# Performance work log

Hardware: AMD Instinct MI355X
Metric: run time of the kernel (lower is better)

The kernel has to match this reference:

```python
import math
import jax, jax.numpy as jnp
import numpy as np

B, S, E, H = 2, 2048, 1024, 16
D = E // H  # head_dim = 64
NEG = jnp.float32(-1e9)  # finite stand-in for masked_fill(-inf) to avoid NaN in attn @ V


def setup_inputs() -> dict:
    key = jax.random.key(0)
    ks = jax.random.split(key, 8)
    inp = {
        "query": jax.random.normal(ks[0], (B, S, E), jnp.float32),
        "key": jax.random.normal(ks[1], (B, S, E), jnp.float32),
        "value": jax.random.normal(ks[2], (B, S, E), jnp.float32),
        "Wq": jax.random.normal(ks[3], (E, E), jnp.float32) * 0.02,
        "bq": jnp.zeros((E,), jnp.float32),
        "Wk": jax.random.normal(ks[4], (E, E), jnp.float32) * 0.02,
        "bk": jnp.zeros((E,), jnp.float32),
        "Wv": jax.random.normal(ks[5], (E, E), jnp.float32) * 0.02,
        "bv": jnp.zeros((E,), jnp.float32),
        "pos_bias": jax.random.normal(ks[6], (H, 2 * S - 1), jnp.float32) * 0.02,
    }
    # gather indices: per-head row index [H,1,1] and relative-position index [S,S]
    inp["idx0"] = jnp.arange(H, dtype=jnp.int32).reshape(H, 1, 1)
    rel = np.arange(S)[:, None] - np.arange(S)[None, :] + (S - 1)  # in [0, 2S-2]
    inp["idx1"] = jnp.asarray(rel, jnp.int32)
    # causal boolean mask: True where masked (j > i)
    inp["mask"] = jnp.triu(jnp.ones((S, S), jnp.bool_), k=1)
    return inp


def _split(x):  # [B,S,E] -> [B,H,S,D]
    return x.reshape(B, S, H, D).transpose(0, 2, 1, 3)


def reference(query, key, value, Wq, bq, Wk, bk, Wv, bv, pos_bias, idx0, idx1, mask):
    q = _split(query @ Wq.T + bq)
    k = _split(key @ Wk.T + bk)
    v = _split(value @ Wv.T + bv)
    logits = jnp.einsum("bhqd,bhkd->bhqk", q, k) / math.sqrt(D)  # [B,H,S,S]
    logits = logits + pos_bias[idx0, idx1]  # gather -> [H,S,S], broadcast over B
    logits = jnp.where(mask, NEG, logits)   # masked_fill
    attn = jax.nn.log_softmax(logits, axis=-1)  # module uses LogSoftmax (faithful)
    out = jnp.einsum("bhqk,bhkd->bhqd", attn, v)
    return out.transpose(0, 2, 1, 3).reshape(B, S, E)
```

## Files before the change

### kernel.cpp

```cpp
#include <hip/hip_runtime.h>
#include <math.h>

constexpr int BB = 2;
constexpr int SS = 2048;
constexpr int EE = 1024;
constexpr int HH = 16;
constexpr int DD = 64;
constexpr int NSEG = 32;

typedef short short8 __attribute__((ext_vector_type(8)));
typedef short short4_t __attribute__((ext_vector_type(4)));
typedef float floatx4 __attribute__((ext_vector_type(4)));
typedef unsigned short ushort_t;

__device__ __forceinline__ ushort_t f2bf(float f) {
    unsigned int u = __float_as_uint(f);
    u += 0x7fffu + ((u >> 16) & 1u);
    return (ushort_t)(u >> 16);
}

__device__ __forceinline__ void gl_lds16(const void* g, void* l) {
    __builtin_amdgcn_global_load_lds(
        (const __attribute__((address_space(1))) void*)g,
        (__attribute__((address_space(3))) void*)l, 16, 0, 0);
}

__global__ __launch_bounds__(256) void repack_kernel(
    const float* __restrict__ s0, const float* __restrict__ s1, const float* __restrict__ s2,
    ushort_t* __restrict__ dst, int rows)
{
    const float* src = (blockIdx.z == 0) ? s0 : (blockIdx.z == 1) ? s1 : s2;
    ushort_t* d = dst + (size_t)blockIdx.z * rows * EE;
    const int idx = blockIdx.x * 256 + threadIdx.x;
    const int row = idx >> 7;
    const int gir = idx & 127;
    const int blk = gir >> 3, g = gir & 7;
    const int gp = g ^ (row & 7);
    const float* sp = src + (size_t)row * EE + gir * 8;
    float4 a = *(const float4*)sp;
    float4 b = *(const float4*)(sp + 4);
    short8 o;
    o[0] = (short)f2bf(a.x); o[1] = (short)f2bf(a.y); o[2] = (short)f2bf(a.z); o[3] = (short)f2bf(a.w);
    o[4] = (short)f2bf(b.x); o[5] = (short)f2bf(b.y); o[6] = (short)f2bf(b.z); o[7] = (short)f2bf(b.w);
    *(short8*)&d[(size_t)row * EE + blk * 64 + gp * 8] = o;
}

__global__ __launch_bounds__(256) void proj_kernel(
    const ushort_t* __restrict__ Xall, const ushort_t* __restrict__ Wall,
    const float* __restrict__ bq, const float* __restrict__ bk, const float* __restrict__ bv,
    ushort_t* __restrict__ qb, ushort_t* __restrict__ kbb,
    float* __restrict__ vf, ushort_t* __restrict__ vtb)
{
    __shared__ __align__(16) ushort_t Xs[128 * 64];
    __shared__ __align__(16) ushort_t Ws[128 * 64];

    const int z = blockIdx.z;
    const ushort_t* X = Xall + (size_t)z * BB * SS * EE;
    const ushort_t* W = Wall + (size_t)z * EE * EE;
    const float* bias = (z == 0) ? bq : (z == 1) ? bk : bv;

    const int t = threadIdx.x, w = t >> 6, l = t & 63, ln = t & 15, qd = (t >> 4) & 3;
    const int row0 = blockIdx.x * 128;
    const int col0 = blockIdx.y * 128;
    const int wzm = (w & 1) * 64, wzn = (w >> 1) * 64;

    floatx4 acc[4][4];
    #pragma unroll
    for (int i = 0; i < 4; ++i)
        #pragma unroll
        for (int j = 0; j < 4; ++j)
            acc[i][j] = (floatx4){0.f, 0.f, 0.f, 0.f};

    for (int k0 = 0; k0 < EE; k0 += 64) {
        __syncthreads();
        #pragma unroll
        for (int j = 0; j < 4; ++j) {
            const int c = w * 4 + j;
            const int r = c * 8 + (l >> 3);
            gl_lds16(&X[(size_t)(row0 + r) * EE + k0 + (l & 7) * 8], &Xs[c * 512]);
            gl_lds16(&W[(size_t)(col0 + r) * EE + k0 + (l & 7) * 8], &Ws[c * 512]);
        }
        __syncthreads();

        const ushort_t* Am = (z < 2) ? Ws : Xs;
        const ushort_t* Bn = (z < 2) ? Xs : Ws;
        #pragma unroll
        for (int kh = 0; kh < 2; ++kh) {
            const int sw = ((kh * 4 + qd) ^ (ln & 7)) * 8;
            short8 af[4], bfr[4];
            #pragma unroll
            for (int mi = 0; mi < 4; ++mi)
                af[mi] = *(const short8*)&Am[(wzm + mi * 16 + ln) * 64 + sw];
            #pragma unroll
            for (int ni = 0; ni < 4; ++ni)
                bfr[ni] = *(const short8*)&Bn[(wzn + ni * 16 + ln) * 64 + sw];
            #pragma unroll
            for (int mi = 0; mi < 4; ++mi)
                #pragma unroll
                for (int ni = 0; ni < 4; ++ni)
                    acc[mi][ni] = __builtin_amdgcn_mfma_f32_16x16x32_bf16(af[mi], bfr[ni], acc[mi][ni], 0, 0, 0);
        }
    }

    if (z < 2) {
        ushort_t* dst = z ? kbb : qb;
        #pragma unroll
        for (int mi = 0; mi < 4; ++mi) {
            const int o0 = col0 + wzm + mi * 16 + qd * 4;
            const float4 b4 = *(const float4*)&bias[o0];
            const int h = o0 >> 6, d0 = o0 & 63;
            const int g = d0 >> 3, dlow = d0 & 7;
            #pragma unroll
            for (int ni = 0; ni < 4; ++ni) {
                const int s = row0 + wzn + ni * 16 + ln;
                const int b = s >> 11, sr = s & (SS - 1);
                const int gp = g ^ (sr & 7);
                short4_t pk;
                pk[0] = (short)f2bf(acc[mi][ni][0] + b4.x);
                pk[1] = (short)f2bf(acc[mi][ni][1] + b4.y);
                pk[2] = (short)f2bf(acc[mi][ni][2] + b4.z);
                pk[3] = (short)f2bf(acc[mi][ni][3] + b4.w);
                *(short4_t*)&dst[((size_t)((b * HH + h) * SS) + sr) * DD + gp * 8 + dlow] = pk;
            }
        }
    } else {
        #pragma unroll
        for (int mi = 0; mi < 4; ++mi) {
            const int s0 = row0 + wzm + mi * 16 + qd * 4;
            const int b = s0 >> 11, sr0 = s0 & (SS - 1);
            const int sg = (sr0 >> 3) & 7, slow = sr0 & 7;
            #pragma unroll
            for (int ni = 0; ni < 4; ++ni) {
                const int o = col0 + wzn + ni * 16 + ln;
                const int h = o >> 6, d = o & 63;
                const float bvv = bias[o];
                float v0 = acc[mi][ni][0] + bvv, v1 = acc[mi][ni][1] + bvv;
                float v2 = acc[mi][ni][2] + bvv, v3 = acc[mi][ni][3] + bvv;
                float* vp = &vf[((size_t)((b * HH + h) * SS) + sr0) * DD + d];
                vp[0 * DD] = v0; vp[1 * DD] = v1; vp[2 * DD] = v2; vp[3 * DD] = v3;
                const int gp2 = sg ^ (d & 7);
                short4_t pk;
                pk[0] = (short)f2bf(v0); pk[1] = (short)f2bf(v1);
                pk[2] = (short)f2bf(v2); pk[3] = (short)f2bf(v3);
                *(short4_t*)&vtb[((size_t)((b * HH + h) * DD) + d) * SS + (sr0 & ~63) + gp2 * 8 + slow] = pk;
            }
        }
    }
}

__global__ __launch_bounds__(64) void scan_partial(
    const float* __restrict__ v, float* __restrict__ Sv, float* __restrict__ segsum)
{
    const int blk = blockIdx.x;
    const int seg = blk & (NSEG - 1);
    const int bh  = blk >> 5;
    const int d   = threadIdx.x;
    const float* vp = v  + ((size_t)bh * SS + seg * 64) * DD + d;
    float*       sp = Sv + ((size_t)bh * SS + seg * 64) * DD + d;
    float run = 0.f;
    for (int s = 63; s >= 0; --s) { sp[s * DD] = run; run += vp[s * DD]; }
    segsum[(size_t)(bh * NSEG + seg) * DD + d] = run;
}

__global__ __launch_bounds__(64) void scan_finalize(
    float* __restrict__ Sv, const float* __restrict__ segsum, float* __restrict__ Tot)
{
    const int blk = blockIdx.x;
    const int seg = blk & (NSEG - 1);
    const int bh  = blk >> 5;
    const int d   = threadIdx.x;
    float off = 0.f;
    for (int c = seg + 1; c < NSEG; ++c)
        off += segsum[(size_t)(bh * NSEG + c) * DD + d];
    float* sp = Sv + ((size_t)bh * SS + seg * 64) * DD + d;
    for (int s = 0; s < 64; ++s) sp[s * DD] += off;
    if (seg == 0)
        Tot[bh * DD + d] = off + segsum[(size_t)(bh * NSEG) * DD + d];
}

__global__ __launch_bounds__(256) void attn_kernel(
    const ushort_t* __restrict__ qb, const ushort_t* __restrict__ kbb,
    const ushort_t* __restrict__ vtb, const float* __restrict__ Sv,
    const float* __restrict__ Tot, const float* __restrict__ pb,
    float* __restrict__ out)
{
    __shared__ __align__(16) ushort_t Ks[2][64 * 64];
    __shared__ __align__(16) ushort_t Vt[2][64 * 64];
    __shared__ __align__(16) ushort_t Ls[128 * 72];
    __shared__ float pbL[2048];

    const int t = threadIdx.x, w = t >> 6, l = t & 63, ln = t & 15, qd = (t >> 4) & 3;
    const int id = blockIdx.x, bh = id & 31, tt = id >> 5;
    const int qt = (tt < 8) ? (15 - tt) : (tt - 8);
    const int b = bh >> 4, h = bh & 15, i0 = qt * 128;

    {
        const float* p = pb + h * (2 * SS - 1) + (SS - 1);
        *(float4*)&pbL[t * 8]     = *(const float4*)&p[t * 8];
        *(float4*)&pbL[t * 8 + 4] = *(const float4*)&p[t * 8 + 4];
    }

    short8 qf[2][2];
    #pragma unroll
    for (int mt = 0; mt < 2; ++mt)
        #pragma unroll
        for (int kh = 0; kh < 2; ++kh) {
            const int i = i0 + 32 * w + 16 * mt + ln;
            qf[mt][kh] = *(const short8*)&qb[((size_t)bh * SS + i) * DD + (((kh * 4 + qd) ^ (ln & 7)) * 8)];
        }

    floatx4 accpv[2][4];
    #pragma unroll
    for (int mt = 0; mt < 2; ++mt)
        #pragma unroll
        for (int ct = 0; ct < 4; ++ct)
            accpv[mt][ct] = (floatx4){0.f, 0.f, 0.f, 0.f};
    float part[2][4] = {};

    const int nkt = 2 * qt + 2;

    auto stage = [&](int buf, int kt) {
        const int k0 = kt * 64;
        #pragma unroll
        for (int j = 0; j < 2; ++j) {
            const int c = w * 2 + j;
            const int rk = c * 8 + (l >> 3);
            gl_lds16(&kbb[((size_t)bh * SS + k0 + rk) * DD + (l & 7) * 8], &Ks[buf][c * 512]);
            gl_lds16(&vtb[((size_t)bh * DD + rk) * SS + k0 + (l & 7) * 8], &Vt[buf][c * 512]);
        }
    };

    stage(0, 0);
    for (int kt = 0; kt < nkt; ++kt) {
        __syncthreads();
        if (kt + 1 < nkt) stage((kt + 1) & 1, kt + 1);
        const ushort_t* KsC = Ks[kt & 1];
        const ushort_t* VtC = Vt[kt & 1];
        const int k0 = kt * 64;

        floatx4 aq[2][4];
        #pragma unroll
        for (int mt = 0; mt < 2; ++mt)
            #pragma unroll
            for (int ct = 0; ct < 4; ++ct)
                aq[mt][ct] = (floatx4){0.f, 0.f, 0.f, 0.f};
        #pragma unroll
        for (int kh = 0; kh < 2; ++kh) {
            const int sw = ((kh * 4 + qd) ^ (ln & 7)) * 8;
            short8 bfr[4];
            #pragma unroll
            for (int ct = 0; ct < 4; ++ct)
                bfr[ct] = *(const short8*)&KsC[(ct * 16 + ln) * 64 + sw];
            #pragma unroll
            for (int mt = 0; mt < 2; ++mt)
                #pragma unroll
                for (int ct = 0; ct < 4; ++ct)
                    aq[mt][ct] = __builtin_amdgcn_mfma_f32_16x16x32_bf16(qf[mt][kh], bfr[ct], aq[mt][ct], 0, 0, 0);
        }

        const int kdiag = i0 - k0;
        if (kt < 2 * qt) {
            #pragma unroll
            for (int mt = 0; mt < 2; ++mt)
                #pragma unroll
                for (int ct = 0; ct < 4; ++ct) {
                    const int krel = ct * 16 + ln;
                    #pragma unroll
                    for (int reg = 0; reg < 4; ++reg) {
                        const int irel = 32 * w + 16 * mt + qd * 4 + reg;
                        const float val = aq[mt][ct][reg] * 0.125f + pbL[kdiag + irel - krel];
                        part[mt][reg] += __expf(val);
                        Ls[irel * 72 + krel] = f2bf(val);
                    }
                }
        } else {
            #pragma unroll
            for (int mt = 0; mt < 2; ++mt)
                #pragma unroll
                for (int ct = 0; ct < 4; ++ct) {
                    const int krel = ct * 16 + ln;
                    #pragma unroll
                    for (int reg = 0; reg < 4; ++reg) {
                        const int irel = 32 * w + 16 * mt + qd * 4 + reg;
                        const int rel = kdiag + irel - krel;
                        const bool ok = rel >= 0;
                        const float val = aq[mt][ct][reg] * 0.125f + pbL[ok ? rel : 0];
                        part[mt][reg] += ok ? __expf(val) : 0.f;
                        Ls[irel * 72 + krel] = ok ? f2bf(val) : (ushort_t)0;
                    }
                }
        }

        #pragma unroll
        for (int kh = 0; kh < 2; ++kh) {
            const int sw = ((kh * 4 + qd) ^ (ln & 7)) * 8;
            short8 af[2], bfr[4];
            #pragma unroll
            for (int mt = 0; mt < 2; ++mt)
                af[mt] = *(const short8*)&Ls[(32 * w + 16 * mt + ln) * 72 + kh * 32 + qd * 8];
            #pragma unroll
            for (int ct = 0; ct < 4; ++ct)
                bfr[ct] = *(const short8*)&VtC[(ct * 16 + ln) * 64 + sw];
            #pragma unroll
            for (int mt = 0; mt < 2; ++mt)
                #pragma unroll
                for (int ct = 0; ct < 4; ++ct)
                    accpv[mt][ct] = __builtin_amdgcn_mfma_f32_16x16x32_bf16(af[mt], bfr[ct], accpv[mt][ct], 0, 0, 0);
        }
    }

    float lse[2][4];
    #pragma unroll
    for (int mt = 0; mt < 2; ++mt)
        #pragma unroll
        for (int reg = 0; reg < 4; ++reg) {
            float p = part[mt][reg];
            p += __shfl_xor(p, 1, 64);
            p += __shfl_xor(p, 2, 64);
            p += __shfl_xor(p, 4, 64);
            p += __shfl_xor(p, 8, 64);
            lse[mt][reg] = __logf(p);
        }

    float tot[4];
    #pragma unroll
    for (int ct = 0; ct < 4; ++ct) tot[ct] = Tot[bh * DD + ct * 16 + ln];

    #pragma unroll
    for (int mt = 0; mt < 2; ++mt)
        #pragma unroll
        for (int ct = 0; ct < 4; ++ct) {
            const int d = ct * 16 + ln;
            #pragma unroll
            for (int reg = 0; reg < 4; ++reg) {
                const int ig = i0 + 32 * w + 16 * mt + qd * 4 + reg;
                const float sv = Sv[((size_t)bh * SS + ig) * DD + d];
                const float o = accpv[mt][ct][reg] - lse[mt][reg] * tot[ct] - 1e9f * sv;
                out[((size_t)(b * SS + ig)) * EE + h * DD + d] = o;
            }
        }
}

extern "C" void kernel_launch(void* const* d_in, const int* in_sizes, int n_in,
                              void* d_out, int out_size, void* d_ws, size_t ws_size,
                              hipStream_t stream)
{
    const float* query = (const float*)d_in[0];
    const float* key_  = (const float*)d_in[1];
    const float* value = (const float*)d_in[2];
    const float* Wq = (const float*)d_in[3];
    const float* bq = (const float*)d_in[4];
    const float* Wk = (const float*)d_in[5];
    const float* bk = (const float*)d_in[6];
    const float* Wv = (const float*)d_in[7];
    const float* bv = (const float*)d_in[8];
    const float* pb = (const float*)d_in[9];
    float* out = (float*)d_out;

    float* ws = (float*)d_ws;
    const size_t SZ = (size_t)BB * SS * EE;
    float* vf   = ws;
    float* Svb  = ws + SZ;
    float* Totb = ws + 2 * SZ;
    float* segs = Totb + BB * HH * DD;
    ushort_t* us  = (ushort_t*)(segs + (size_t)BB * HH * NSEG * DD);
    ushort_t* qbp = us;
    ushort_t* kbp = qbp + SZ;
    ushort_t* vtp = kbp + SZ;
    ushort_t* Xbf = vtp + SZ;
    ushort_t* Wbf = Xbf + 3 * SZ;

    repack_kernel<<<dim3((unsigned)(SZ / 8 / 256), 1, 3), 256, 0, stream>>>(
        query, key_, value, Xbf, BB * SS);
    repack_kernel<<<dim3((unsigned)((size_t)EE * EE / 8 / 256), 1, 3), 256, 0, stream>>>(
        Wq, Wk, Wv, Wbf, EE);

    proj_kernel<<<dim3(BB * SS / 128, EE / 128, 3), 256, 0, stream>>>(
        Xbf, Wbf, bq, bk, bv, qbp, kbp, vf, vtp);

    scan_partial<<<BB * HH * NSEG, 64, 0, stream>>>(vf, Svb, segs);
    scan_finalize<<<BB * HH * NSEG, 64, 0, stream>>>(Svb, segs, Totb);

    attn_kernel<<<BB * HH * (SS / 128), 256, 0, stream>>>(
        qbp, kbp, vtp, Svb, Totb, pb, out);
}
```

Before: 258.2 us.

## Merge repack launches, drop fp32 V copy, rebuild scan, widen attention blocks

Folds the two repack launches into one kernel, stops writing the fp32 V tensor and instead computes the suffix-sum scan from the bf16 transposed V with a parallel two-kernel scan. The attention kernel moves to 512 threads with one 16-row tile per wave, skips fully masked key tiles per wave, and packs bf16 logits in pairs via DPP/perm for 32-bit LDS stores with a padded stride. This targets launch overhead, fp32 traffic and the serial scan, while raising attention occupancy. The catch is that the scan now reads bf16-rounded V, which slightly changes the -1e9*Sv term's precision.

```diff
diff --git a/kernel.cpp b/kernel.cpp
--- a/kernel.cpp
+++ b/kernel.cpp
@@ -6,7 +6,6 @@
 constexpr int EE = 1024;
 constexpr int HH = 16;
 constexpr int DD = 64;
-constexpr int NSEG = 32;
 
 typedef short short8 __attribute__((ext_vector_type(8)));
 typedef short short4_t __attribute__((ext_vector_type(4)));
@@ -18,6 +17,9 @@
     u += 0x7fffu + ((u >> 16) & 1u);
     return (ushort_t)(u >> 16);
 }
+__device__ __forceinline__ float bf2f(short s) {
+    return __uint_as_float(((unsigned)(ushort_t)s) << 16);
+}
 
 __device__ __forceinline__ void gl_lds16(const void* g, void* l) {
     __builtin_amdgcn_global_load_lds(
@@ -25,31 +27,42 @@
         (__attribute__((address_space(3))) void*)l, 16, 0, 0);
 }
 
-__global__ __launch_bounds__(256) void repack_kernel(
-    const float* __restrict__ s0, const float* __restrict__ s1, const float* __restrict__ s2,
-    ushort_t* __restrict__ dst, int rows)
-{
-    const float* src = (blockIdx.z == 0) ? s0 : (blockIdx.z == 1) ? s1 : s2;
-    ushort_t* d = dst + (size_t)blockIdx.z * rows * EE;
+__global__ __launch_bounds__(256) void repack_all(
+    const float* __restrict__ x0, const float* __restrict__ x1, const float* __restrict__ x2,
+    const float* __restrict__ w0, const float* __restrict__ w1, const float* __restrict__ w2,
+    ushort_t* __restrict__ Xbf, ushort_t* __restrict__ Wbf)
+{
     const int idx = blockIdx.x * 256 + threadIdx.x;
     const int row = idx >> 7;
     const int gir = idx & 127;
+    const float* src;
+    ushort_t* dst;
+    int r;
+    if (row < 3 * BB * SS) {
+        const int z = row >> 12; r = row & (BB * SS - 1);
+        src = (z == 0) ? x0 : (z == 1) ? x1 : x2;
+        dst = Xbf + (size_t)z * BB * SS * EE;
+    } else {
+        const int rw = row - 3 * BB * SS;
+        const int z = rw >> 10; r = rw & (EE - 1);
+        src = (z == 0) ? w0 : (z == 1) ? w1 : w2;
+        dst = Wbf + (size_t)z * EE * EE;
+    }
     const int blk = gir >> 3, g = gir & 7;
-    const int gp = g ^ (row & 7);
-    const float* sp = src + (size_t)row * EE + gir * 8;
+    const int gp = g ^ (r & 7);
+    const float* sp = src + (size_t)r * EE + gir * 8;
     float4 a = *(const float4*)sp;
     float4 b = *(const float4*)(sp + 4);
     short8 o;
     o[0] = (short)f2bf(a.x); o[1] = (short)f2bf(a.y); o[2] = (short)f2bf(a.z); o[3] = (short)f2bf(a.w);
     o[4] = (short)f2bf(b.x); o[5] = (short)f2bf(b.y); o[6] = (short)f2bf(b.z); o[7] = (short)f2bf(b.w);
-    *(short8*)&d[(size_t)row * EE + blk * 64 + gp * 8] = o;
+    *(short8*)&dst[(size_t)r * EE + blk * 64 + gp * 8] = o;
 }
 
 __global__ __launch_bounds__(256) void proj_kernel(
     const ushort_t* __restrict__ Xall, const ushort_t* __restrict__ Wall,
     const float* __restrict__ bq, const float* __restrict__ bk, const float* __restrict__ bv,
-    ushort_t* __restrict__ qb, ushort_t* __restrict__ kbb,
-    float* __restrict__ vf, ushort_t* __restrict__ vtb)
+    ushort_t* __restrict__ qb, ushort_t* __restrict__ kbb, ushort_t* __restrict__ vtb)
 {
     __shared__ __align__(16) ushort_t Xs[128 * 64];
     __shared__ __align__(16) ushort_t Ws[128 * 64];
@@ -134,51 +147,71 @@
                 const int o = col0 + wzn + ni * 16 + ln;
                 const int h = o >> 6, d = o & 63;
                 const float bvv = bias[o];
-                float v0 = acc[mi][ni][0] + bvv, v1 = acc[mi][ni][1] + bvv;
-                float v2 = acc[mi][ni][2] + bvv, v3 = acc[mi][ni][3] + bvv;
-                float* vp = &vf[((size_t)((b * HH + h) * SS) + sr0) * DD + d];
-                vp[0 * DD] = v0; vp[1 * DD] = v1; vp[2 * DD] = v2; vp[3 * DD] = v3;
                 const int gp2 = sg ^ (d & 7);
                 short4_t pk;
-                pk[0] = (short)f2bf(v0); pk[1] = (short)f2bf(v1);
-                pk[2] = (short)f2bf(v2); pk[3] = (short)f2bf(v3);
+                pk[0] = (short)f2bf(acc[mi][ni][0] + bvv);
+                pk[1] = (short)f2bf(acc[mi][ni][1] + bvv);
+                pk[2] = (short)f2bf(acc[mi][ni][2] + bvv);
+                pk[3] = (short)f2bf(acc[mi][ni][3] + bvv);
                 *(short4_t*)&vtb[((size_t)((b * HH + h) * DD) + d) * SS + (sr0 & ~63) + gp2 * 8 + slow] = pk;
             }
         }
     }
 }
 
-__global__ __launch_bounds__(64) void scan_partial(
-    const float* __restrict__ v, float* __restrict__ Sv, float* __restrict__ segsum)
-{
-    const int blk = blockIdx.x;
-    const int seg = blk & (NSEG - 1);
-    const int bh  = blk >> 5;
-    const int d   = threadIdx.x;
-    const float* vp = v  + ((size_t)bh * SS + seg * 64) * DD + d;
-    float*       sp = Sv + ((size_t)bh * SS + seg * 64) * DD + d;
-    float run = 0.f;
-    for (int s = 63; s >= 0; --s) { sp[s * DD] = run; run += vp[s * DD]; }
-    segsum[(size_t)(bh * NSEG + seg) * DD + d] = run;
-}
-
-__global__ __launch_bounds__(64) void scan_finalize(
-    float* __restrict__ Sv, const float* __restrict__ segsum, float* __restrict__ Tot)
-{
-    const int blk = blockIdx.x;
-    const int seg = blk & (NSEG - 1);
-    const int bh  = blk >> 5;
-    const int d   = threadIdx.x;
-    float off = 0.f;
-    for (int c = seg + 1; c < NSEG; ++c)
-        off += segsum[(size_t)(bh * NSEG + c) * DD + d];
-    float* sp = Sv + ((size_t)bh * SS + seg * 64) * DD + d;
-    for (int s = 0; s < 64; ++s) sp[s * DD] += off;
-    if (seg == 0)
-        Tot[bh * DD + d] = off + segsum[(size_t)(bh * NSEG) * DD + d];
-}
-
-__global__ __launch_bounds__(256) void attn_kernel(
+__global__ __launch_bounds__(256) void scan_chunks(
+    const ushort_t* __restrict__ vtb, float* __restrict__ segs)
+{
+    const int t = threadIdx.x;
+    const int d = blockIdx.x * 8 + (t >> 5);
+    const int ch = t & 31;
+    const int bh = blockIdx.y;
+    const ushort_t* src = vtb + ((size_t)(bh * DD + d)) * SS + ch * 64;
+    float s = 0.f;
+    #pragma unroll
+    for (int i = 0; i < 8; ++i) {
+        short8 v = *(const short8*)&src[i * 8];
+        #pragma unroll
+        for (int j = 0; j < 8; ++j) s += bf2f(v[j]);
+    }
+    segs[((size_t)(bh * DD + d)) * 32 + ch] = s;
+}
+
+__global__ __launch_bounds__(256) void scan_finalize(
+    const ushort_t* __restrict__ vtb, const float* __restrict__ segs,
+    float* __restrict__ Sv, float* __restrict__ Tot)
+{
+    __shared__ float offp[4][64], subs[4][64];
+    const int t = threadIdx.x, dd = t & 63, j = t >> 6;
+    const int c = blockIdx.x, bh = blockIdx.y;
+
+    float o = 0.f;
+    for (int c2 = c + 1 + j; c2 < 32; c2 += 4)
+        o += segs[((size_t)(bh * DD + dd)) * 32 + c2];
+    offp[j][dd] = o;
+
+    const ushort_t* vrow = vtb + ((size_t)(bh * DD + dd)) * SS + c * 64;
+    const int g0 = (2 * j) ^ (dd & 7), g1 = (2 * j + 1) ^ (dd & 7);
+    short8 a0 = *(const short8*)&vrow[g0 * 8];
+    short8 a1 = *(const short8*)&vrow[g1 * 8];
+    float arr[16];
+    #pragma unroll
+    for (int i = 0; i < 8; ++i) { arr[i] = bf2f(a0[i]); arr[8 + i] = bf2f(a1[i]); }
+    float sub = 0.f;
+    #pragma unroll
+    for (int i = 0; i < 16; ++i) sub += arr[i];
+    subs[j][dd] = sub;
+    __syncthreads();
+
+    float run = offp[0][dd] + offp[1][dd] + offp[2][dd] + offp[3][dd];
+    for (int j2 = j + 1; j2 < 4; ++j2) run += subs[j2][dd];
+
+    float* svp = Sv + ((size_t)bh * SS + c * 64 + j * 16) * DD + dd;
+    for (int s = 15; s >= 0; --s) { svp[s * DD] = run; run += arr[s]; }
+    if (c == 0 && j == 0) Tot[bh * DD + dd] = run;
+}
+
+__global__ __launch_bounds__(512, 4) void attn_kernel(
     const ushort_t* __restrict__ qb, const ushort_t* __restrict__ kbb,
     const ushort_t* __restrict__ vtb, const float* __restrict__ Sv,
     const float* __restrict__ Tot, const float* __restrict__ pb,
@@ -186,48 +219,37 @@
 {
     __shared__ __align__(16) ushort_t Ks[2][64 * 64];
     __shared__ __align__(16) ushort_t Vt[2][64 * 64];
-    __shared__ __align__(16) ushort_t Ls[128 * 72];
+    __shared__ __align__(16) ushort_t Ls[128 * 76];
     __shared__ float pbL[2048];
 
     const int t = threadIdx.x, w = t >> 6, l = t & 63, ln = t & 15, qd = (t >> 4) & 3;
     const int id = blockIdx.x, bh = id & 31, tt = id >> 5;
     const int qt = (tt < 8) ? (15 - tt) : (tt - 8);
     const int b = bh >> 4, h = bh & 15, i0 = qt * 128;
+    const int r0 = 16 * w;
 
     {
         const float* p = pb + h * (2 * SS - 1) + (SS - 1);
-        *(float4*)&pbL[t * 8]     = *(const float4*)&p[t * 8];
-        *(float4*)&pbL[t * 8 + 4] = *(const float4*)&p[t * 8 + 4];
-    }
-
-    short8 qf[2][2];
-    #pragma unroll
-    for (int mt = 0; mt < 2; ++mt)
-        #pragma unroll
-        for (int kh = 0; kh < 2; ++kh) {
-            const int i = i0 + 32 * w + 16 * mt + ln;
-            qf[mt][kh] = *(const short8*)&qb[((size_t)bh * SS + i) * DD + (((kh * 4 + qd) ^ (ln & 7)) * 8)];
-        }
-
-    floatx4 accpv[2][4];
-    #pragma unroll
-    for (int mt = 0; mt < 2; ++mt)
-        #pragma unroll
-        for (int ct = 0; ct < 4; ++ct)
-            accpv[mt][ct] = (floatx4){0.f, 0.f, 0.f, 0.f};
-    float part[2][4] = {};
+        *(float4*)&pbL[t * 4] = *(const float4*)&p[t * 4];
+    }
+
+    short8 qf[2];
+    #pragma unroll
+    for (int kh = 0; kh < 2; ++kh)
+        qf[kh] = *(const short8*)&qb[((size_t)bh * SS + i0 + r0 + ln) * DD + (((kh * 4 + qd) ^ (ln & 7)) * 8)];
+
+    floatx4 accpv[4];
+    #pragma unroll
+    for (int ct = 0; ct < 4; ++ct) accpv[ct] = (floatx4){0.f, 0.f, 0.f, 0.f};
+    float part[4] = {};
 
     const int nkt = 2 * qt + 2;
 
     auto stage = [&](int buf, int kt) {
         const int k0 = kt * 64;
-        #pragma unroll
-        for (int j = 0; j < 2; ++j) {
-            const int c = w * 2 + j;
-            const int rk = c * 8 + (l >> 3);
-            gl_lds16(&kbb[((size_t)bh * SS + k0 + rk) * DD + (l & 7) * 8], &Ks[buf][c * 512]);
-            gl_lds16(&vtb[((size_t)bh * DD + rk) * SS + k0 + (l & 7) * 8], &Vt[buf][c * 512]);
-        }
+        const int row = w * 8 + (l >> 3), cg = l & 7;
+        gl_lds16(&kbb[((size_t)bh * SS + k0 + row) * DD + cg * 8], &Ks[buf][w * 512]);
+        gl_lds16(&vtb[((size_t)bh * DD + row) * SS + k0 + cg * 8], &Vt[buf][w * 512]);
     };
 
     stage(0, 0);
@@ -236,109 +258,93 @@
         if (kt + 1 < nkt) stage((kt + 1) & 1, kt + 1);
         const ushort_t* KsC = Ks[kt & 1];
         const ushort_t* VtC = Vt[kt & 1];
-        const int k0 = kt * 64;
-
-        floatx4 aq[2][4];
-        #pragma unroll
-        for (int mt = 0; mt < 2; ++mt)
-            #pragma unroll
-            for (int ct = 0; ct < 4; ++ct)
-                aq[mt][ct] = (floatx4){0.f, 0.f, 0.f, 0.f};
+        const int k0 = kt * 64, kdiag = i0 - k0;
+
+        if (kdiag + r0 + 15 < 0) continue;
+
+        floatx4 aq[4];
+        #pragma unroll
+        for (int ct = 0; ct < 4; ++ct) aq[ct] = (floatx4){0.f, 0.f, 0.f, 0.f};
         #pragma unroll
         for (int kh = 0; kh < 2; ++kh) {
             const int sw = ((kh * 4 + qd) ^ (ln & 7)) * 8;
-            short8 bfr[4];
-            #pragma unroll
-            for (int ct = 0; ct < 4; ++ct)
-                bfr[ct] = *(const short8*)&KsC[(ct * 16 + ln) * 64 + sw];
-            #pragma unroll
-            for (int mt = 0; mt < 2; ++mt)
-                #pragma unroll
-                for (int ct = 0; ct < 4; ++ct)
-                    aq[mt][ct] = __builtin_amdgcn_mfma_f32_16x16x32_bf16(qf[mt][kh], bfr[ct], aq[mt][ct], 0, 0, 0);
-        }
-
-        const int kdiag = i0 - k0;
-        if (kt < 2 * qt) {
-            #pragma unroll
-            for (int mt = 0; mt < 2; ++mt)
-                #pragma unroll
-                for (int ct = 0; ct < 4; ++ct) {
-                    const int krel = ct * 16 + ln;
-                    #pragma unroll
-                    for (int reg = 0; reg < 4; ++reg) {
-                        const int irel = 32 * w + 16 * mt + qd * 4 + reg;
-                        const float val = aq[mt][ct][reg] * 0.125f + pbL[kdiag + irel - krel];
-                        part[mt][reg] += __expf(val);
-                        Ls[irel * 72 + krel] = f2bf(val);
-                    }
+            #pragma unroll
+            for (int ct = 0; ct < 4; ++ct) {
+                short8 bfr = *(const short8*)&KsC[(ct * 16 + ln) * 64 + sw];
+                aq[ct] = __builtin_amdgcn_mfma_f32_16x16x32_bf16(qf[kh], bfr, aq[ct], 0, 0, 0);
+            }
+        }
+
+        const int irel0 = r0 + qd * 4;
+        unsigned* Ld = (unsigned*)Ls;
+        const bool unmasked = (kt < 2 * qt);
+        #pragma unroll
+        for (int ct = 0; ct < 4; ++ct) {
+            const int krel = ct * 16 + ln;
+            const int pbase = kdiag + irel0 - krel;
+            unsigned pk[4];
+            #pragma unroll
+            for (int reg = 0; reg < 4; ++reg) {
+                unsigned u;
+                if (unmasked) {
+                    const float val = aq[ct][reg] * 0.125f + pbL[pbase + reg];
+                    part[reg] += __expf(val);
+                    u = __float_as_uint(val);
+                } else {
+                    const int rel = pbase + reg;
+                    const bool ok = rel >= 0;
+                    const float val = aq[ct][reg] * 0.125f + pbL[ok ? rel : 0];
+                    part[reg] += ok ? __expf(val) : 0.f;
+                    u = ok ? __float_as_uint(val) : 0u;
                 }
-        } else {
-            #pragma unroll
-            for (int mt = 0; mt < 2; ++mt)
-                #pragma unroll
-                for (int ct = 0; ct < 4; ++ct) {
-                    const int krel = ct * 16 + ln;
-                    #pragma unroll
-                    for (int reg = 0; reg < 4; ++reg) {
-                        const int irel = 32 * w + 16 * mt + qd * 4 + reg;
-                        const int rel = kdiag + irel - krel;
-                        const bool ok = rel >= 0;
-                        const float val = aq[mt][ct][reg] * 0.125f + pbL[ok ? rel : 0];
-                        part[mt][reg] += ok ? __expf(val) : 0.f;
-                        Ls[irel * 72 + krel] = ok ? f2bf(val) : (ushort_t)0;
-                    }
-                }
+                const unsigned nb = (unsigned)__builtin_amdgcn_mov_dpp((int)u, 0xF5, 0xF, 0xF, false);
+                pk[reg] = __builtin_amdgcn_perm(nb, u, 0x07060302);
+            }
+            if (!(ln & 1)) {
+                const int base = irel0 * 38 + (krel >> 1);
+                Ld[base] = pk[0]; Ld[base + 38] = pk[1];
+                Ld[base + 76] = pk[2]; Ld[base + 114] = pk[3];
+            }
         }
 
         #pragma unroll
         for (int kh = 0; kh < 2; ++kh) {
+            short8 af = *(const short8*)&Ls[(r0 + ln) * 76 + kh * 32 + qd * 8];
             const int sw = ((kh * 4 + qd) ^ (ln & 7)) * 8;
-            short8 af[2], bfr[4];
-            #pragma unroll
-            for (int mt = 0; mt < 2; ++mt)
-                af[mt] = *(const short8*)&Ls[(32 * w + 16 * mt + ln) * 72 + kh * 32 + qd * 8];
-            #pragma unroll
-            for (int ct = 0; ct < 4; ++ct)
-                bfr[ct] = *(const short8*)&VtC[(ct * 16 + ln) * 64 + sw];
-            #pragma unroll
-            for (int mt = 0; mt < 2; ++mt)
-                #pragma unroll
-                for (int ct = 0; ct < 4; ++ct)
-                    accpv[mt][ct] = __builtin_amdgcn_mfma_f32_16x16x32_bf16(af[mt], bfr[ct], accpv[mt][ct], 0, 0, 0);
-        }
-    }
-
-    float lse[2][4];
-    #pragma unroll
-    for (int mt = 0; mt < 2; ++mt)
+            #pragma unroll
+            for (int ct = 0; ct < 4; ++ct) {
+                short8 bfr = *(const short8*)&VtC[(ct * 16 + ln) * 64 + sw];
+                accpv[ct] = __builtin_amdgcn_mfma_f32_16x16x32_bf16(af, bfr, accpv[ct], 0, 0, 0);
+            }
+        }
+    }
+
+    float lse[4];
+    #pragma unroll
+    for (int reg = 0; reg < 4; ++reg) {
+        float p = part[reg];
+        p += __shfl_xor(p, 1, 64);
+        p += __shfl_xor(p, 2, 64);
+        p += __shfl_xor(p, 4, 64);
+        p += __shfl_xor(p, 8, 64);
+        lse[reg] = __logf(p);
+    }
+
+    float tot[4];
+    #pragma unroll
+    for (int ct = 0; ct < 4; ++ct) tot[ct] = Tot[bh * DD + ct * 16 + ln];
+
+    #pragma unroll
+    for (int ct = 0; ct < 4; ++ct) {
+        const int d = ct * 16 + ln;
         #pragma unroll
         for (int reg = 0; reg < 4; ++reg) {
-            float p = part[mt][reg];
-            p += __shfl_xor(p, 1, 64);
-            p += __shfl_xor(p, 2, 64);
-            p += __shfl_xor(p, 4, 64);
-            p += __shfl_xor(p, 8, 64);
-            lse[mt][reg] = __logf(p);
-        }
-
-    float tot[4];
-    #pragma unroll
-    for (int ct = 0; ct < 4; ++ct) tot[ct] = Tot[bh * DD + ct * 16 + ln];
-
-    #pragma unroll
-    for (int mt = 0; mt < 2; ++mt)
-        #pragma unroll
-        for (int ct = 0; ct < 4; ++ct) {
-            const int d = ct * 16 + ln;
-            #pragma unroll
-            for (int reg = 0; reg < 4; ++reg) {
-                const int ig = i0 + 32 * w + 16 * mt + qd * 4 + reg;
-                const float sv = Sv[((size_t)bh * SS + ig) * DD + d];
-                const float o = accpv[mt][ct][reg] - lse[mt][reg] * tot[ct] - 1e9f * sv;
-                out[((size_t)(b * SS + ig)) * EE + h * DD + d] = o;
-            }
-        }
+            const int ig = i0 + r0 + qd * 4 + reg;
+            const float sv = Sv[((size_t)bh * SS + ig) * DD + d];
+            const float o = accpv[ct][reg] - lse[reg] * tot[ct] - 1e9f * sv;
+            out[((size_t)(b * SS + ig)) * EE + h * DD + d] = o;
+        }
+    }
 }
 
 extern "C" void kernel_launch(void* const* d_in, const int* in_sizes, int n_in,
@@ -359,28 +365,25 @@
 
     float* ws = (float*)d_ws;
     const size_t SZ = (size_t)BB * SS * EE;
-    float* vf   = ws;
-    float* Svb  = ws + SZ;
-    float* Totb = ws + 2 * SZ;
-    float* segs = Totb + BB * HH * DD;
-    ushort_t* us  = (ushort_t*)(segs + (size_t)BB * HH * NSEG * DD);
+    float* Svb  = ws;
+    float* Totb = ws + SZ;
+    float* segs = Totb + (size_t)BB * HH * DD;
+    ushort_t* us  = (ushort_t*)(segs + (size_t)BB * HH * DD * 32);
     ushort_t* qbp = us;
     ushort_t* kbp = qbp + SZ;
     ushort_t* vtp = kbp + SZ;
     ushort_t* Xbf = vtp + SZ;
     ushort_t* Wbf = Xbf + 3 * SZ;
 
-    repack_kernel<<<dim3((unsigned)(SZ / 8 / 256), 1, 3), 256, 0, stream>>>(
-        query, key_, value, Xbf, BB * SS);
-    repack_kernel<<<dim3((unsigned)((size_t)EE * EE / 8 / 256), 1, 3), 256, 0, stream>>>(
-        Wq, Wk, Wv, Wbf, EE);
+    const int ngroups = (3 * BB * SS + 3 * EE) * (EE / 8);
+    repack_all<<<ngroups / 256, 256, 0, stream>>>(query, key_, value, Wq, Wk, Wv, Xbf, Wbf);
 
     proj_kernel<<<dim3(BB * SS / 128, EE / 128, 3), 256, 0, stream>>>(
-        Xbf, Wbf, bq, bk, bv, qbp, kbp, vf, vtp);
-
-    scan_partial<<<BB * HH * NSEG, 64, 0, stream>>>(vf, Svb, segs);
-    scan_finalize<<<BB * HH * NSEG, 64, 0, stream>>>(Svb, segs, Totb);
-
-    attn_kernel<<<BB * HH * (SS / 128), 256, 0, stream>>>(
+        Xbf, Wbf, bq, bk, bv, qbp, kbp, vtp);
+
+    scan_chunks<<<dim3(8, BB * HH), 256, 0, stream>>>(vtp, segs);
+    scan_finalize<<<dim3(32, BB * HH), 256, 0, stream>>>(vtp, segs, Svb, Totb);
+
+    attn_kernel<<<BB * HH * (SS / 128), 512, 0, stream>>>(
         qbp, kbp, vtp, Svb, Totb, pb, out);
 }
```

After: 260.2 us. No clear change (+0.8%).
